# Optimization experiments

Measured on AMD Instinct MI355X. Metric: run time of the kernel, lower is better.

Reference implementation:

```python
import jax, jax.numpy as jnp
import numpy as np

DT = 1.0 / 200.0  # imu_freq = 200
EPS = 1e-8

def _skew(v):  # [B,3] -> [B,3,3]
    x, y, z = v[:, 0], v[:, 1], v[:, 2]
    zero = jnp.zeros_like(x)
    return jnp.stack([zero, -z, y, z, zero, -x, -y, x, zero], axis=-1).reshape(-1, 3, 3)

def _axis_angle_to_R(w, dt):
    # Rodrigues: R = I + sin(th) K + (1-cos(th)) K^2, th = ||w||*dt
    n = jnp.linalg.norm(w, axis=-1, keepdims=True)          # [B,1]
    theta = n[:, 0] * dt                                     # [B]
    axis = w / (n + EPS)
    K = _skew(axis)
    I = jnp.eye(3, dtype=w.dtype)
    s = jnp.sin(theta)[:, None, None]
    c = jnp.cos(theta)[:, None, None]
    return I + s * K + (1.0 - c) * jnp.einsum('bij,bjk->bik', K, K)

def _R_to_axis_angle(R):
    tr = jnp.trace(R, axis1=-2, axis2=-1)
    angle = jnp.arccos(jnp.clip((tr - 1.0) / 2.0, -1.0 + 1e-7, 1.0 - 1e-7))
    axis = jnp.stack([R[:, 2, 1] - R[:, 1, 2],
                      R[:, 0, 2] - R[:, 2, 0],
                      R[:, 1, 0] - R[:, 0, 1]], axis=-1)
    axis = axis / (2.0 * jnp.sin(angle)[:, None] + EPS)
    return axis, angle

def _aa_to_quat(axis, angle):  # (w, x, y, z)
    h = angle / 2.0
    return jnp.concatenate([jnp.cos(h)[:, None], axis * jnp.sin(h)[:, None]], axis=-1)

def setup_inputs() -> dict:
    key = jax.random.key(0)
    input_seq = jax.random.normal(key, (512, 4096, 6), dtype=jnp.float32)
    return {"input_seq": input_seq}

def reference(input_seq):
    B, T, _ = input_seq.shape
    dtype = input_seq.dtype
    w = jnp.transpose(input_seq[:, :, :3], (1, 0, 2))  # [T,B,3] gyro
    a = jnp.transpose(input_seq[:, :, 3:], (1, 0, 2))  # [T,B,3] accel
    dt = jnp.asarray(DT, dtype)
    dt2_half = dt * dt / 2.0

    dR0 = jnp.broadcast_to(jnp.eye(3, dtype=dtype), (B, 3, 3))
    dv0 = jnp.zeros((B, 3), dtype)
    dp0 = jnp.zeros((B, 3), dtype)

    def step(carry, inp):
        dR, dv, dp = carry
        w_k, a_k = inp
        dR = jnp.einsum('bij,bjk->bik', dR, _axis_angle_to_R(w_k, dt))
        Ra = jnp.einsum('bij,bj->bi', dR, a_k)
        dv = dv + Ra * dt
        dp = dp + dv * dt + Ra * dt2_half  # uses already-updated dv, as in torch code
        axis, angle = _R_to_axis_angle(dR)
        q = _aa_to_quat(axis, angle)
        return (dR, dv, dp), (dp, dv, q)

    _, (ps, vs, qs) = jax.lax.scan(step, (dR0, dv0, dp0), (w, a))
    ps = jnp.transpose(ps, (1, 0, 2))  # [B,T,3]
    vs = jnp.transpose(vs, (1, 0, 2))  # [B,T,3]
    qs = jnp.transpose(qs, (1, 0, 2))  # [B,T,4]
    return jnp.concatenate([input_seq, ps, qs, vs], axis=2)  # [B,T,16]
```

## Files before the change

### kernel.cpp

```cpp
#include <hip/hip_runtime.h>
#include <math.h>

#define T_LEN 4096
#define CHUNK 8
#define NTHR  512
#define NWAVE (NTHR / 64)

typedef float f32x4 __attribute__((ext_vector_type(4)));

__device__ __forceinline__ void make_A(float wx, float wy, float wz, float* A) {
    const float dt  = 1.0f / 200.0f;
    const float dt2 = dt * dt;
    float n2 = wx*wx + wy*wy + wz*wz;
    float t2 = n2 * dt2;
    float s_ = dt  * (1.0f + t2 * (-1.0f/6.0f  + t2 * (1.0f/120.0f)));
    float oc = dt2 * (0.5f + t2 * (-1.0f/24.0f + t2 * (1.0f/720.0f)));
    float xx = wx*wx, yy = wy*wy, zz = wz*wz;
    float xy = wx*wy, xz = wx*wz, yz = wy*wz;
    A[0] = 1.0f - oc*(yy+zz);
    A[1] = -s_*wz + oc*xy;
    A[2] =  s_*wy + oc*xz;
    A[3] =  s_*wz + oc*xy;
    A[4] = 1.0f - oc*(xx+zz);
    A[5] = -s_*wx + oc*yz;
    A[6] = -s_*wy + oc*xz;
    A[7] =  s_*wx + oc*yz;
    A[8] = 1.0f - oc*(xx+yy);
}

__device__ __forceinline__ void matmul3(const float* R, const float* A, float* N) {
#pragma unroll
    for (int i = 0; i < 3; ++i) {
        N[i*3+0] = R[i*3+0]*A[0] + R[i*3+1]*A[3] + R[i*3+2]*A[6];
        N[i*3+1] = R[i*3+0]*A[1] + R[i*3+1]*A[4] + R[i*3+2]*A[7];
        N[i*3+2] = R[i*3+0]*A[2] + R[i*3+1]*A[5] + R[i*3+2]*A[8];
    }
}

__device__ __forceinline__ void step(float* E, float wx, float wy, float wz,
                                     float ax, float ay, float az) {
    const float dt   = 1.0f / 200.0f;
    const float dt2h = dt * dt * 0.5f;
    float A[9], N[9];
    make_A(wx, wy, wz, A);
    matmul3(E, A, N);
#pragma unroll
    for (int i = 0; i < 9; ++i) E[i] = N[i];
    float rax = E[0]*ax + E[1]*ay + E[2]*az;
    float ray = E[3]*ax + E[4]*ay + E[5]*az;
    float raz = E[6]*ax + E[7]*ay + E[8]*az;
    E[9]  += rax*dt; E[10] += ray*dt; E[11] += raz*dt;
    E[12] += E[9]*dt  + rax*dt2h;
    E[13] += E[10]*dt + ray*dt2h;
    E[14] += E[11]*dt + raz*dt2h;
}

__device__ __forceinline__ void compose(const float* __restrict__ L,
                                        float* __restrict__ e, float tauY) {
    float N[9];
    matmul3(L, e, N);
    float b0 = L[9]  + L[0]*e[9] + L[1]*e[10] + L[2]*e[11];
    float b1 = L[10] + L[3]*e[9] + L[4]*e[10] + L[5]*e[11];
    float b2 = L[11] + L[6]*e[9] + L[7]*e[10] + L[8]*e[11];
    float c0 = L[12] + tauY*L[9]  + L[0]*e[12] + L[1]*e[13] + L[2]*e[14];
    float c1 = L[13] + tauY*L[10] + L[3]*e[12] + L[4]*e[13] + L[5]*e[14];
    float c2 = L[14] + tauY*L[11] + L[6]*e[12] + L[7]*e[13] + L[8]*e[14];
#pragma unroll
    for (int i = 0; i < 9; ++i) e[i] = N[i];
    e[9]  = b0; e[10] = b1; e[11] = b2;
    e[12] = c0; e[13] = c1; e[14] = c2;
}

__device__ __forceinline__ float4 quat_of(const float* S) {
    float tr = S[0] + S[4] + S[8];
    float ca = fminf(fmaxf(0.5f * (tr - 1.0f), -1.0f + 1e-7f), 1.0f - 1e-7f);
    float x  = 0.5f * (1.0f + ca);
    float r  = __frsqrt_rn(x);
    float qw = x * r;
    float i4 = 0.25f * r;
    return make_float4(qw, (S[7] - S[5]) * i4,
                           (S[2] - S[6]) * i4,
                           (S[3] - S[1]) * i4);
}

__global__ __launch_bounds__(NTHR, 2)
void preint_kernel(const float* __restrict__ in, float* __restrict__ out) {
    const int b    = blockIdx.x;
    const int t    = threadIdx.x;
    const int lane = t & 63;
    const int w    = t >> 6;
    const float dt = 1.0f / 200.0f;

    const float* bin  = in  + (size_t)b * T_LEN * 6;
    float*       bout = out + (size_t)b * T_LEN * 16;
    const float4* src4 = (const float4*)(bin + (size_t)t * CHUNK * 6);

    __shared__ __align__(16) float4 tile[NTHR * 8];
    float* wtot = (float*)tile;

    float4 u[12];
#pragma unroll
    for (int i = 0; i < 12; ++i) u[i] = src4[i];
    __builtin_amdgcn_sched_barrier(0);

    float e[15] = {1,0,0, 0,1,0, 0,0,1, 0,0,0, 0,0,0};
#pragma unroll
    for (int pp = 0; pp < CHUNK / 2; ++pp) {
        float4 u0 = u[pp*3+0];
        float4 u1 = u[pp*3+1];
        float4 u2 = u[pp*3+2];
        step(e, u0.x, u0.y, u0.z, u0.w, u1.x, u1.y);
        step(e, u1.z, u1.w, u2.x, u2.y, u2.z, u2.w);
    }

#pragma unroll
    for (int d = 1; d < 64; d <<= 1) {
        float L[15];
#pragma unroll
        for (int i = 0; i < 15; ++i) L[i] = __shfl_up(e[i], d, 64);
        if (lane >= d) compose(L, e, (float)(d * CHUNK) * dt);
    }

    if (lane == 63) {
#pragma unroll
        for (int i = 0; i < 15; ++i) wtot[w*15 + i] = e[i];
    }
    __syncthreads();

    if (w == 0) {
        float s[15] = {1,0,0, 0,1,0, 0,0,1, 0,0,0, 0,0,0};
        if (lane < NWAVE) {
#pragma unroll
            for (int i = 0; i < 15; ++i) s[i] = wtot[lane*15 + i];
        }
#pragma unroll
        for (int d = 1; d < NWAVE; d <<= 1) {
            float L[15];
#pragma unroll
            for (int i = 0; i < 15; ++i) L[i] = __shfl_up(s[i], d, 64);
            if (lane >= d && lane < NWAVE)
                compose(L, s, (float)(d * 64 * CHUNK) * dt);
        }
        if (lane < NWAVE) {
#pragma unroll
            for (int i = 0; i < 15; ++i) wtot[lane*15 + i] = s[i];
        }
    }
    __syncthreads();

    float st[15];
#pragma unroll
    for (int i = 0; i < 15; ++i) st[i] = __shfl_up(e[i], 1, 64);
    if (lane == 0) {
        st[0]=1; st[1]=0; st[2]=0; st[3]=0; st[4]=1; st[5]=0;
        st[6]=0; st[7]=0; st[8]=1; st[9]=0; st[10]=0; st[11]=0;
        st[12]=0; st[13]=0; st[14]=0;
    }
    {
        float P[15] = {1,0,0, 0,1,0, 0,0,1, 0,0,0, 0,0,0};
        if (w > 0) {
#pragma unroll
            for (int i = 0; i < 15; ++i) P[i] = wtot[(w-1)*15 + i];
        }
        compose(P, st, (float)(lane * CHUNK) * dt);
    }
    __syncthreads();

    const float4* src4b;
    {
        unsigned long long pbits = (unsigned long long)src4;
        asm volatile("" : "+v"(pbits) : "v"(st[0]), "v"(st[14]));
        src4b = (const float4*)pbits;
    }
    __builtin_amdgcn_sched_barrier(0);

    float4 v[12];
#pragma unroll
    for (int i = 0; i < 12; ++i) v[i] = src4b[i];
    __builtin_amdgcn_sched_barrier(0);

    float4* wt  = tile + (size_t)w * 512;
    f32x4*  go4 = (f32x4*)bout + (size_t)w * 2048;
    const int swz = lane & 7;

#pragma unroll
    for (int pp = 0; pp < CHUNK / 2; ++pp) {
        float4 u0 = v[pp*3+0];
        float4 u1 = v[pp*3+1];
        float4 u2 = v[pp*3+2];

        step(st, u0.x, u0.y, u0.z, u0.w, u1.x, u1.y);
        {
            float4 q = quat_of(st);
            wt[(lane*8 + 0) ^ swz] = make_float4(u0.x, u0.y, u0.z, u0.w);
            wt[(lane*8 + 1) ^ swz] = make_float4(u1.x, u1.y, st[12], st[13]);
            wt[(lane*8 + 2) ^ swz] = make_float4(st[14], q.x, q.y, q.z);
            wt[(lane*8 + 3) ^ swz] = make_float4(q.w, st[9], st[10], st[11]);
        }

        step(st, u1.z, u1.w, u2.x, u2.y, u2.z, u2.w);
        {
            float4 q = quat_of(st);
            wt[(lane*8 + 4) ^ swz] = make_float4(u1.z, u1.w, u2.x, u2.y);
            wt[(lane*8 + 5) ^ swz] = make_float4(u2.z, u2.w, st[12], st[13]);
            wt[(lane*8 + 6) ^ swz] = make_float4(st[14], q.x, q.y, q.z);
            wt[(lane*8 + 7) ^ swz] = make_float4(q.w, st[9], st[10], st[11]);
        }

        asm volatile("s_waitcnt lgkmcnt(0)" ::: "memory");
        __builtin_amdgcn_sched_barrier(0);

#pragma unroll
        for (int i = 0; i < 8; ++i) {
            int c = i*64 + lane;
            float4 x = wt[c ^ ((c >> 3) & 7)];
            f32x4 vv = { x.x, x.y, x.z, x.w };
            int g = i*256 + (lane >> 3)*32 + pp*8 + (lane & 7);
            __builtin_nontemporal_store(vv, &go4[g]);
        }
        __builtin_amdgcn_sched_barrier(0);
    }
}

extern "C" void kernel_launch(void* const* d_in, const int* in_sizes, int n_in,
                              void* d_out, int out_size, void* d_ws, size_t ws_size,
                              hipStream_t stream) {
    const float* in = (const float*)d_in[0];
    float* out = (float*)d_out;
    const int B = in_sizes[0] / (T_LEN * 6);
    preint_kernel<<<dim3(B), dim3(NTHR), 0, stream>>>(in, out);
}
```

Measured before the change: 182.6 us.

## Split scan into segment-totals and emit kernels with 64-thread blocks

Replaces the single 512-thread-per-batch kernel with two launches. The first computes each 512-step segment's composed transform per wave and writes it to workspace. The second recomputes local prefixes and serially composes the preceding segment totals before emitting outputs. This removes block-level syncthreads and the cross-wave scan, and gives finer-grained blocks for scheduling. The cost is reading the input twice more, recomputing the local scan, an extra launch, and up to 7 serial composes per block.

```diff
diff --git a/kernel.cpp b/kernel.cpp
--- a/kernel.cpp
+++ b/kernel.cpp
@@ -3,8 +3,9 @@
 
 #define T_LEN 4096
 #define CHUNK 8
-#define NTHR  512
-#define NWAVE (NTHR / 64)
+#define WTHR  64
+#define SEG   (WTHR * CHUNK)
+#define NSEG  (T_LEN / SEG)
 
 typedef float f32x4 __attribute__((ext_vector_type(4)));
 
@@ -83,70 +84,73 @@
                            (S[3] - S[1]) * i4);
 }
 
-__global__ __launch_bounds__(NTHR, 2)
-void preint_kernel(const float* __restrict__ in, float* __restrict__ out) {
-    const int b    = blockIdx.x;
-    const int t    = threadIdx.x;
-    const int lane = t & 63;
-    const int w    = t >> 6;
+__global__ __launch_bounds__(WTHR)
+void totals_kernel(const float* __restrict__ in, float* __restrict__ ws) {
+    const int g    = blockIdx.x;
+    const int lane = threadIdx.x;
     const float dt = 1.0f / 200.0f;
 
-    const float* bin  = in  + (size_t)b * T_LEN * 6;
-    float*       bout = out + (size_t)b * T_LEN * 16;
-    const float4* src4 = (const float4*)(bin + (size_t)t * CHUNK * 6);
-
-    __shared__ __align__(16) float4 tile[NTHR * 8];
-    float* wtot = (float*)tile;
-
+    const float4* src4 = (const float4*)(in +
+        ((size_t)g * SEG + (size_t)lane * CHUNK) * 6);
     float4 u[12];
 #pragma unroll
     for (int i = 0; i < 12; ++i) u[i] = src4[i];
-    __builtin_amdgcn_sched_barrier(0);
 
     float e[15] = {1,0,0, 0,1,0, 0,0,1, 0,0,0, 0,0,0};
 #pragma unroll
     for (int pp = 0; pp < CHUNK / 2; ++pp) {
-        float4 u0 = u[pp*3+0];
-        float4 u1 = u[pp*3+1];
-        float4 u2 = u[pp*3+2];
+        float4 u0 = u[pp*3+0], u1 = u[pp*3+1], u2 = u[pp*3+2];
         step(e, u0.x, u0.y, u0.z, u0.w, u1.x, u1.y);
         step(e, u1.z, u1.w, u2.x, u2.y, u2.z, u2.w);
     }
 
 #pragma unroll
     for (int d = 1; d < 64; d <<= 1) {
+        float R[15];
+#pragma unroll
+        for (int i = 0; i < 15; ++i) R[i] = __shfl_down(e[i], d, 64);
+        compose(e, R, (float)(d * CHUNK) * dt);
+#pragma unroll
+        for (int i = 0; i < 15; ++i) e[i] = R[i];
+    }
+    if (lane == 0) {
+#pragma unroll
+        for (int i = 0; i < 15; ++i) ws[(size_t)g * 15 + i] = e[i];
+    }
+}
+
+__global__ __launch_bounds__(WTHR)
+void emit_kernel(const float* __restrict__ in, const float* __restrict__ ws,
+                 float* __restrict__ out) {
+    const int g    = blockIdx.x;
+    const int s    = g & (NSEG - 1);
+    const int lane = threadIdx.x;
+    const float dt = 1.0f / 200.0f;
+
+    const float4* src4 = (const float4*)(in +
+        ((size_t)g * SEG + (size_t)lane * CHUNK) * 6);
+
+    __shared__ __align__(16) float4 wt[512];
+
+    float4 u[12];
+#pragma unroll
+    for (int i = 0; i < 12; ++i) u[i] = src4[i];
+
+    float e[15] = {1,0,0, 0,1,0, 0,0,1, 0,0,0, 0,0,0};
+#pragma unroll
+    for (int pp = 0; pp < CHUNK / 2; ++pp) {
+        float4 u0 = u[pp*3+0], u1 = u[pp*3+1], u2 = u[pp*3+2];
+        step(e, u0.x, u0.y, u0.z, u0.w, u1.x, u1.y);
+        step(e, u1.z, u1.w, u2.x, u2.y, u2.z, u2.w);
+    }
+
+#pragma unroll
+    for (int d = 1; d < 64; d <<= 1) {
         float L[15];
 #pragma unroll
         for (int i = 0; i < 15; ++i) L[i] = __shfl_up(e[i], d, 64);
         if (lane >= d) compose(L, e, (float)(d * CHUNK) * dt);
     }
-
-    if (lane == 63) {
-#pragma unroll
-        for (int i = 0; i < 15; ++i) wtot[w*15 + i] = e[i];
-    }
-    __syncthreads();
-
-    if (w == 0) {
-        float s[15] = {1,0,0, 0,1,0, 0,0,1, 0,0,0, 0,0,0};
-        if (lane < NWAVE) {
-#pragma unroll
-            for (int i = 0; i < 15; ++i) s[i] = wtot[lane*15 + i];
-        }
-#pragma unroll
-        for (int d = 1; d < NWAVE; d <<= 1) {
-            float L[15];
-#pragma unroll
-            for (int i = 0; i < 15; ++i) L[i] = __shfl_up(s[i], d, 64);
-            if (lane >= d && lane < NWAVE)
-                compose(L, s, (float)(d * 64 * CHUNK) * dt);
-        }
-        if (lane < NWAVE) {
-#pragma unroll
-            for (int i = 0; i < 15; ++i) wtot[lane*15 + i] = s[i];
-        }
-    }
-    __syncthreads();
 
     float st[15];
 #pragma unroll
@@ -156,15 +160,23 @@
         st[6]=0; st[7]=0; st[8]=1; st[9]=0; st[10]=0; st[11]=0;
         st[12]=0; st[13]=0; st[14]=0;
     }
+
     {
-        float P[15] = {1,0,0, 0,1,0, 0,0,1, 0,0,0, 0,0,0};
-        if (w > 0) {
-#pragma unroll
-            for (int i = 0; i < 15; ++i) P[i] = wtot[(w-1)*15 + i];
-        }
-        compose(P, st, (float)(lane * CHUNK) * dt);
-    }
-    __syncthreads();
+        float P0[15] = {1,0,0, 0,1,0, 0,0,1, 0,0,0, 0,0,0};
+#pragma unroll
+        for (int k = 0; k < NSEG - 1; ++k) {
+            if (k < s) {
+                float tmp[15];
+                const float* Tk = ws + (size_t)(g - s + k) * 15;
+#pragma unroll
+                for (int i = 0; i < 15; ++i) tmp[i] = Tk[i];
+                compose(P0, tmp, (float)SEG * dt);
+#pragma unroll
+                for (int i = 0; i < 15; ++i) P0[i] = tmp[i];
+            }
+        }
+        compose(P0, st, (float)(lane * CHUNK) * dt);
+    }
 
     const float4* src4b;
     {
@@ -179,15 +191,12 @@
     for (int i = 0; i < 12; ++i) v[i] = src4b[i];
     __builtin_amdgcn_sched_barrier(0);
 
-    float4* wt  = tile + (size_t)w * 512;
-    f32x4*  go4 = (f32x4*)bout + (size_t)w * 2048;
+    f32x4* go4 = (f32x4*)out + (size_t)g * (SEG * 4);
     const int swz = lane & 7;
 
 #pragma unroll
     for (int pp = 0; pp < CHUNK / 2; ++pp) {
-        float4 u0 = v[pp*3+0];
-        float4 u1 = v[pp*3+1];
-        float4 u2 = v[pp*3+2];
+        float4 u0 = v[pp*3+0], u1 = v[pp*3+1], u2 = v[pp*3+2];
 
         step(st, u0.x, u0.y, u0.z, u0.w, u1.x, u1.y);
         {
@@ -197,7 +206,6 @@
             wt[(lane*8 + 2) ^ swz] = make_float4(st[14], q.x, q.y, q.z);
             wt[(lane*8 + 3) ^ swz] = make_float4(q.w, st[9], st[10], st[11]);
         }
-
         step(st, u1.z, u1.w, u2.x, u2.y, u2.z, u2.w);
         {
             float4 q = quat_of(st);
@@ -215,8 +223,8 @@
             int c = i*64 + lane;
             float4 x = wt[c ^ ((c >> 3) & 7)];
             f32x4 vv = { x.x, x.y, x.z, x.w };
-            int g = i*256 + (lane >> 3)*32 + pp*8 + (lane & 7);
-            __builtin_nontemporal_store(vv, &go4[g]);
+            int gi = i*256 + (lane >> 3)*32 + pp*8 + (lane & 7);
+            __builtin_nontemporal_store(vv, &go4[gi]);
         }
         __builtin_amdgcn_sched_barrier(0);
     }
@@ -227,6 +235,9 @@
                               hipStream_t stream) {
     const float* in = (const float*)d_in[0];
     float* out = (float*)d_out;
+    float* ws  = (float*)d_ws;
     const int B = in_sizes[0] / (T_LEN * 6);
-    preint_kernel<<<dim3(B), dim3(NTHR), 0, stream>>>(in, out);
-}
+    const int G = B * NSEG;
+    totals_kernel<<<dim3(G), dim3(WTHR), 0, stream>>>(in, ws);
+    emit_kernel<<<dim3(G), dim3(WTHR), 0, stream>>>(in, ws, out);
+}
```

Result: slower. 191.4 us (+4.8%).
